# Optimization experiments

Measured on AMD Instinct MI355X. Metric: run time of the kernel, lower is better.

## Reference

```python
import jax, jax.numpy as jnp
import numpy as np

K = 5          # number of neighbors (topk k=5+1, drop self)
EPS = 1e-05    # hparams['epsilon'] for gentropy term


def setup_inputs() -> dict:
    key = jax.random.key(0)
    k1, k2, k3, k4, k5 = jax.random.split(key, 5)
    B, D, C, N = 256, 256, 64, 200000
    features = jax.random.normal(k1, (B, D), dtype=jnp.float32)
    W = jax.random.normal(k2, (D, C), dtype=jnp.float32) * 0.05
    b = jnp.zeros((C,), dtype=jnp.float32)
    fea_bank = jax.random.normal(k3, (N, D), dtype=jnp.float32)
    # score bank holds softmax outputs -> make rows valid probability distributions
    score_bank = jax.nn.softmax(jax.random.normal(k4, (N, C), dtype=jnp.float32), axis=-1)
    trg_idx = jax.random.randint(k5, (B,), 0, N, dtype=jnp.int64)
    return {"features": features, "W": W, "b": b,
            "fea_bank": fea_bank, "score_bank": score_bank, "trg_idx": trg_idx}


def reference(features, W, b, fea_bank, score_bank, trg_idx):
    sg = jax.lax.stop_gradient
    B = features.shape[0]
    C = W.shape[1]

    logits = features @ W + b                       # classifier(features)
    softmax_out = jax.nn.softmax(logits, axis=-1)   # [B, C] (differentiable)

    # --- everything bank-related is under torch.no_grad in the original ---
    nrm = jnp.maximum(jnp.linalg.norm(features, axis=1, keepdims=True), 1e-12)
    f_norm = sg(features / nrm)                     # F.normalize(features)
    fb = sg(fea_bank.at[trg_idx].set(f_norm))        # fea_bank[trg_idx] = f_norm
    sb = sg(score_bank.at[trg_idx].set(sg(softmax_out)))

    dist = f_norm @ fb.T                             # [B, N]
    _, idx_near = jax.lax.top_k(dist, K + 1)
    idx_near = idx_near[:, 1:]                       # [B, K] drop self

    score_near = sb[idx_near]                        # [B, K, C]
    fea_near = fb[idx_near]                          # [B, K, D]

    dist2 = jnp.einsum('bkd,nd->bkn', fea_near, fb)  # [B, K, N]
    _, idx_nn = jax.lax.top_k(dist2, K + 1)
    idx_nn = idx_nn[:, :, 1:]                        # [B, K, K]

    match = (idx_nn == trg_idx[:, None, None]).sum(-1).astype(jnp.float32)  # [B, K]
    weight = jnp.where(match > 0.0, match, jnp.float32(0.1))                # [B, K]
    weight_kk = jnp.full((B, K * K), 0.1, dtype=jnp.float32)  # fill_(0.1) overwrites

    score_near_kk = sb[idx_nn].reshape(B, K * K, C)  # [B, K*K, C]
    # --- end no_grad region ---

    # F.kl_div(input, target, reduction='none') = target * (log(target) - input)
    # (original passes probabilities, not log-probs, as input -- kept faithfully)
    kl_kk = score_near_kk * (jnp.log(score_near_kk) - softmax_out[:, None, :])
    loss = jnp.mean((kl_kk.sum(-1) * weight_kk).sum(1))

    kl_n = score_near * (jnp.log(score_near) - softmax_out[:, None, :])
    loss = loss + jnp.mean((kl_n.sum(-1) * weight).sum(1))

    msoftmax = softmax_out.mean(axis=0)
    gentropy = jnp.sum(msoftmax * jnp.log(msoftmax + EPS))
    loss = loss + gentropy
    return loss
```

## Files before the change

kernel.cpp:

```cpp
#include <hip/hip_runtime.h>
#include <hip/hip_bf16.h>
#include <math.h>

#define B_SZ   256
#define D_DIM  256
#define C_DIM  64
#define N_CAND 200000
#define K_TOP  5
#define CHUNK  64
#define NCHGLB (N_CAND / CHUNK)
#define CHUNK_SH 16384
#define NCHJ1  8
#define NCHJ2  16
#define S1     ((NCHGLB + NCHJ1 - 1) / NCHJ1)
#define S2     ((NCHGLB + NCHJ2 - 1) / NCHJ2)

typedef short bf16x8 __attribute__((ext_vector_type(8)));
typedef float f32x16 __attribute__((ext_vector_type(16)));
typedef unsigned short u16x8 __attribute__((ext_vector_type(8)));

__device__ __forceinline__ bool better(float v1, int i1, float v2, int i2) {
    return (v1 > v2) || (v1 == v2 && i1 < i2);
}

__device__ __forceinline__ void insert6f(float* lv, int* li, float v, int idx) {
    if (better(v, idx, lv[5], li[5])) {
        lv[5] = v; li[5] = idx;
        #pragma unroll
        for (int k = 5; k > 0; --k) {
            if (better(lv[k], li[k], lv[k - 1], li[k - 1])) {
                float tv = lv[k]; lv[k] = lv[k - 1]; lv[k - 1] = tv;
                int   ti = li[k]; li[k] = li[k - 1]; li[k - 1] = ti;
            }
        }
    }
}

__device__ __forceinline__ void merge6(const float* av, const int* ai,
                                       const float* bv, const int* bi,
                                       float* ov, int* oi) {
    int ia = 0, ib = 0;
    #pragma unroll
    for (int k = 0; k < 6; ++k) {
        bool ta;
        if (ia >= 6)      ta = false;
        else if (ib >= 6) ta = true;
        else              ta = better(av[ia], ai[ia], bv[ib], bi[ib]);
        if (ta) { ov[k] = av[ia]; oi[k] = ai[ia]; ++ia; }
        else    { ov[k] = bv[ib]; oi[k] = bi[ib]; ++ib; }
    }
}

__device__ __forceinline__ unsigned med3u(unsigned a, unsigned b, unsigned c) {
    unsigned d;
    asm("v_med3_u32 %0, %1, %2, %3" : "=v"(d) : "v"(a), "v"(b), "v"(c));
    return d;
}

__device__ __forceinline__ void kinsert(unsigned* kv, unsigned x) {
    unsigned n0 = kv[0] > x ? kv[0] : x;
    unsigned n1 = med3u(x, kv[0], kv[1]);
    unsigned n2 = med3u(x, kv[1], kv[2]);
    unsigned n3 = med3u(x, kv[2], kv[3]);
    unsigned n4 = med3u(x, kv[3], kv[4]);
    unsigned n5 = med3u(x, kv[4], kv[5]);
    kv[0] = n0; kv[1] = n1; kv[2] = n2; kv[3] = n3; kv[4] = n4; kv[5] = n5;
}

__device__ __forceinline__ unsigned short bf16rne(float x) {
    unsigned int u = __float_as_uint(x);
    unsigned int r = u + 0x7fffu + ((u >> 16) & 1u);
    return (unsigned short)(r >> 16);
}

__device__ __forceinline__ int perm_e(int r, int kk) {
    return ((kk >> 4) * 128) + ((r >> 5) * 64) + (((kk >> 3) & 1) * 32) + (r & 31);
}

__device__ __forceinline__ u16x8 pack8(float4 a, float4 b) {
    u16x8 h;
    h[0] = bf16rne(a.x); h[1] = bf16rne(a.y); h[2] = bf16rne(a.z); h[3] = bf16rne(a.w);
    h[4] = bf16rne(b.x); h[5] = bf16rne(b.y); h[6] = bf16rne(b.z); h[7] = bf16rne(b.w);
    return h;
}

__global__ void k_init(int* pos_of, float* accp) {
    int i = blockIdx.x * 256 + threadIdx.x;
    if (i < N_CAND) pos_of[i] = -1;
    if (i == 0) accp[0] = 0.f;
}

__global__ void k_scatter(const int* __restrict__ trg, int* __restrict__ pos_of) {
    int j = threadIdx.x;
    atomicMax(&pos_of[trg[j]], j);
}

__global__ __launch_bounds__(256) void k_prep(const float* __restrict__ features,
                                              const float* __restrict__ W,
                                              const float* __restrict__ bias,
                                              float* __restrict__ f_norm,
                                              float* __restrict__ softm) {
    int b = blockIdx.x, t = threadIdx.x;
    __shared__ float row[256];
    __shared__ float red[256];
    float x = features[b * D_DIM + t];
    row[t] = x; red[t] = x * x;
    __syncthreads();
    for (int s = 128; s > 0; s >>= 1) {
        if (t < s) red[t] += red[t + s];
        __syncthreads();
    }
    float nrm = fmaxf(sqrtf(red[0]), 1e-12f);
    f_norm[b * D_DIM + t] = x / nrm;
    if (t < C_DIM) {
        float acc = bias[t];
        for (int d = 0; d < D_DIM; ++d) acc = fmaf(row[d], W[d * C_DIM + t], acc);
        float mx = acc;
        for (int off = 32; off > 0; off >>= 1) mx = fmaxf(mx, __shfl_xor(mx, off, 64));
        float e = expf(acc - mx);
        float ssum = e;
        for (int off = 32; off > 0; off >>= 1) ssum += __shfl_xor(ssum, off, 64);
        softm[b * C_DIM + t] = e / ssum;
    }
}

__global__ __launch_bounds__(256) void k_convert(const float* __restrict__ fea_bank,
                                                 const float* __restrict__ f_norm,
                                                 const int* __restrict__ pos_of,
                                                 short* __restrict__ bank) {
    int cc = blockIdx.x, t = threadIdx.x;
    int r = t >> 2, q4 = t & 3;
    int n = cc * CHUNK + r;
    int p = pos_of[n];
    const float* src = (p >= 0) ? (f_norm + (size_t)p * D_DIM)
                                : (fea_bank + (size_t)n * D_DIM);
    short* dst = bank + (size_t)cc * CHUNK_SH;
    #pragma unroll
    for (int i = 0; i < 8; ++i) {
        int kk = q4 * 64 + i * 8;
        float4 a = *(const float4*)(src + kk);
        float4 b = *(const float4*)(src + kk + 4);
        *(u16x8*)(dst + (size_t)perm_e(r, kk) * 8) = pack8(a, b);
    }
}

__global__ __launch_bounds__(256) void k_permq(const float* __restrict__ rows,
                                               const float* __restrict__ fea_bank,
                                               const int* __restrict__ idx,
                                               const int* __restrict__ pos_of,
                                               short* __restrict__ dst) {
    int tile = blockIdx.x, t = threadIdx.x;
    int r = t >> 2, q4 = t & 3;
    const float* src;
    if (idx) {
        int n = idx[tile * 64 + r];
        int p = pos_of[n];
        src = (p >= 0) ? (rows + (size_t)p * D_DIM) : (fea_bank + (size_t)n * D_DIM);
    } else {
        src = rows + (size_t)(tile * 64 + r) * D_DIM;
    }
    short* d = dst + (size_t)tile * CHUNK_SH;
    #pragma unroll
    for (int i = 0; i < 8; ++i) {
        int kk = q4 * 64 + i * 8;
        float4 a = *(const float4*)(src + kk);
        float4 b = *(const float4*)(src + kk + 4);
        *(u16x8*)(d + (size_t)perm_e(r, kk) * 8) = pack8(a, b);
    }
}

__global__ __launch_bounds__(256, 2) void dist_topk(const short* __restrict__ qbf,
                                                    const short* __restrict__ bank,
                                                    float* __restrict__ pval,
                                                    int* __restrict__ pidx,
                                                    int nqt, int swz,
                                                    int S, int nchj) {
    __shared__ __align__(16) short sbuf[2 * CHUNK_SH];

    int slab, qt;
    if (swz) {
        int bid = blockIdx.x;
        int xcd = bid & 7;
        int rem = bid >> 3;
        qt = rem % nqt;
        slab = (rem / nqt) * 8 + xcd;
        if (slab >= S) return;
    } else {
        slab = blockIdx.x;
        qt = blockIdx.y;
    }
    const int cfirst = slab * nchj;
    int nch = NCHGLB - cfirst; if (nch > nchj) nch = nchj;

    const int t   = threadIdx.x;
    const int w   = t >> 6;
    const int l   = t & 63;
    const int khv = l >> 5;
    const int col = l & 31;

    const short* qtile = qbf + (size_t)(qt * 4 + w) * CHUNK_SH;
    bf16x8 bfr0[16], bfr1[16];
    #pragma unroll
    for (int ks = 0; ks < 16; ++ks) {
        bfr0[ks] = *(const bf16x8*)(qtile + (size_t)(ks * 128      + l) * 8);
        bfr1[ks] = *(const bf16x8*)(qtile + (size_t)(ks * 128 + 64 + l) * 8);
    }

    unsigned kv0[6], kv1[6];
    #pragma unroll
    for (int k = 0; k < 6; ++k) { kv0[k] = 0u; kv1[k] = 0u; }

    const short* sbase = bank + (size_t)cfirst * CHUNK_SH;

    #pragma unroll
    for (int i = 0; i < 8; ++i) {
        const short* gp = sbase + (size_t)(i * 256 + t) * 8;
        short* lp = sbuf + (size_t)(i * 256 + w * 64) * 8;
        __builtin_amdgcn_global_load_lds(
            (const __attribute__((address_space(1))) void*)gp,
            (__attribute__((address_space(3))) void*)lp, 16, 0, 0);
    }

    for (int ch = 0; ch < nch; ++ch) {
        const int cur = ch & 1;
        if (ch + 1 < nch) {
            const short* g = sbase + (size_t)(ch + 1) * CHUNK_SH;
            short* lbase = sbuf + (size_t)(cur ^ 1) * CHUNK_SH;
            #pragma unroll
            for (int i = 0; i < 8; ++i) {
                const short* gp = g + (size_t)(i * 256 + t) * 8;
                short* lp = lbase + (size_t)(i * 256 + w * 64) * 8;
                __builtin_amdgcn_global_load_lds(
                    (const __attribute__((address_space(1))) void*)gp,
                    (__attribute__((address_space(3))) void*)lp, 16, 0, 0);
            }
            asm volatile("s_waitcnt vmcnt(8)" ::: "memory");
        } else {
            asm volatile("s_waitcnt vmcnt(0)" ::: "memory");
        }
        __builtin_amdgcn_s_barrier();
        __builtin_amdgcn_sched_barrier(0);

        const short* cb = sbuf + (size_t)cur * CHUNK_SH;

        #pragma unroll
        for (int half = 0; half < 2; ++half) {
            f32x16 a0, a1;
            #pragma unroll
            for (int i = 0; i < 16; ++i) { a0[i] = 2.0f; a1[i] = 2.0f; }
            #pragma unroll
            for (int ks = 0; ks < 16; ++ks) {
                bf16x8 fa = *(const bf16x8*)(cb + (size_t)(ks * 128 + half * 64 + l) * 8);
                a0 = __builtin_amdgcn_mfma_f32_32x32x16_bf16(fa, bfr0[ks], a0, 0, 0, 0);
                a1 = __builtin_amdgcn_mfma_f32_32x32x16_bf16(fa, bfr1[ks], a1, 0, 0, 0);
            }

            const unsigned invb = 511u - (unsigned)(ch * 32 + half * 16);
            #pragma unroll
            for (int r = 0; r < 16; ++r) {
                unsigned x0 = (__float_as_uint(a0[r]) & 0xFFFFFE00u) | (invb - r);
                unsigned x1 = (__float_as_uint(a1[r]) & 0xFFFFFE00u) | (invb - r);
                kinsert(kv0, x0);
                kinsert(kv1, x1);
            }
        }

        __builtin_amdgcn_sched_barrier(0);
        __builtin_amdgcn_s_barrier();
    }

    {
        int q0 = qt * 256 + w * 64 + col;
        int q1 = qt * 256 + w * 64 + 32 + col;
        size_t b0 = ((size_t)q0 * S + slab) * 12 + khv * 6;
        size_t b1 = ((size_t)q1 * S + slab) * 12 + khv * 6;
        #pragma unroll
        for (int k = 0; k < 6; ++k) {
            unsigned key0 = kv0[k], key1 = kv1[k];
            int pos0 = 511 - (int)(key0 & 511u);
            int pos1 = 511 - (int)(key1 & 511u);
            int r0 = pos0 & 15, h0 = (pos0 >> 4) & 1, c0 = pos0 >> 5;
            int r1 = pos1 & 15, h1 = (pos1 >> 4) & 1, c1 = pos1 >> 5;
            int m0 = (r0 & 3) + 8 * (r0 >> 2) + 4 * khv;
            int m1 = (r1 & 3) + 8 * (r1 >> 2) + 4 * khv;
            pval[b0 + k] = __uint_as_float(key0 & 0xFFFFFE00u);
            pidx[b0 + k] = (cfirst + c0) * CHUNK + h0 * 32 + m0;
            pval[b1 + k] = __uint_as_float(key1 & 0xFFFFFE00u);
            pidx[b1 + k] = (cfirst + c1) * CHUNK + h1 * 32 + m1;
        }
    }
}

__global__ __launch_bounds__(256) void topk_merge(const float* __restrict__ pval,
                                                  const int* __restrict__ pidx,
                                                  int* __restrict__ out_idx,
                                                  int S) {
    int q = blockIdx.x, t = threadIdx.x;
    const int total = S * 12;
    float lv[6]; int li[6];
    #pragma unroll
    for (int k = 0; k < 6; ++k) { lv[k] = -3.4e38f; li[k] = 0x7fffffff; }
    size_t base = (size_t)q * total;
    for (int e = t; e < total; e += 256) insert6f(lv, li, pval[base + e], pidx[base + e]);
    __shared__ float sv[256][6];
    __shared__ int   si[256][6];
    #pragma unroll
    for (int k = 0; k < 6; ++k) { sv[t][k] = lv[k]; si[t][k] = li[k]; }
    __syncthreads();
    for (int w = 128; w >= 1; w >>= 1) {
        if (t < w) {
            float ov[6]; int oi[6];
            merge6(sv[t], si[t], sv[t + w], si[t + w], ov, oi);
            #pragma unroll
            for (int k = 0; k < 6; ++k) { sv[t][k] = ov[k]; si[t][k] = oi[k]; }
        }
        __syncthreads();
    }
    if (t == 0) {
        for (int k = 1; k < 6; ++k) out_idx[q * K_TOP + k - 1] = si[0][k];
    }
}

__global__ void k_loss(const float* __restrict__ softm, const float* __restrict__ score_bank,
                       const int* __restrict__ pos_of, const int* __restrict__ idx_near,
                       const int* __restrict__ idx_nn, const int* __restrict__ trg,
                       float* accp) {
    int b = blockIdx.x, c = threadIdx.x;
    float p_bc = softm[b * C_DIM + c];
    float part = 0.f;
    for (int k = 0; k < K_TOP; ++k) {
        for (int j = 0; j < K_TOP; ++j) {
            int n = idx_nn[(b * K_TOP + k) * K_TOP + j];
            int p = pos_of[n];
            const float* srow = (p >= 0) ? (softm + (size_t)p * C_DIM)
                                         : (score_bank + (size_t)n * C_DIM);
            float s = srow[c];
            float v = s * (logf(s) - p_bc);
            for (int off = 32; off > 0; off >>= 1) v += __shfl_down(v, off, 64);
            if (c == 0) part += 0.1f * v;
        }
    }
    for (int k = 0; k < K_TOP; ++k) {
        int n = idx_near[b * K_TOP + k];
        int p = pos_of[n];
        const float* srow = (p >= 0) ? (softm + (size_t)p * C_DIM)
                                     : (score_bank + (size_t)n * C_DIM);
        float s = srow[c];
        float v = s * (logf(s) - p_bc);
        for (int off = 32; off > 0; off >>= 1) v += __shfl_down(v, off, 64);
        if (c == 0) {
            int m = 0;
            for (int j = 0; j < K_TOP; ++j)
                m += (idx_nn[(b * K_TOP + k) * K_TOP + j] == trg[b]) ? 1 : 0;
            float w = (m > 0) ? (float)m : 0.1f;
            part += w * v;
        }
    }
    if (c == 0) atomicAdd(accp, part * (1.0f / (float)B_SZ));
}

__global__ void k_final(const float* __restrict__ softm, const float* __restrict__ accp,
                        float* __restrict__ out) {
    int c = threadIdx.x;
    float m = 0.f;
    for (int b = 0; b < B_SZ; ++b) m += softm[b * C_DIM + c];
    m *= (1.0f / (float)B_SZ);
    float g = m * logf(m + 1e-5f);
    for (int off = 32; off > 0; off >>= 1) g += __shfl_down(g, off, 64);
    if (c == 0) out[0] = accp[0] + g;
}

extern "C" void kernel_launch(void* const* d_in, const int* in_sizes, int n_in,
                              void* d_out, int out_size, void* d_ws, size_t ws_size,
                              hipStream_t stream) {
    const float* features   = (const float*)d_in[0];
    const float* W          = (const float*)d_in[1];
    const float* bias       = (const float*)d_in[2];
    const float* fea_bank   = (const float*)d_in[3];
    const float* score_bank = (const float*)d_in[4];
    const int*   trg        = (const int*)d_in[5];
    float* out = (float*)d_out;

    char* ws = (char*)d_ws;
    size_t off = 0;
    auto alloc = [&](size_t bytes) -> void* {
        void* p = ws + off;
        off = (off + bytes + 255) & ~(size_t)255;
        return p;
    };
    short* bankbf   = (short*)alloc((size_t)NCHGLB * CHUNK_SH * 2);
    short* q1bf     = (short*)alloc((size_t)(B_SZ / 64) * CHUNK_SH * 2);
    short* q2bf     = (short*)alloc((size_t)(B_SZ * K_TOP / 64) * CHUNK_SH * 2);
    float* f_norm   = (float*)alloc((size_t)B_SZ * D_DIM * 4);
    float* softm    = (float*)alloc((size_t)B_SZ * C_DIM * 4);
    int*   pos_of   = (int*)alloc((size_t)N_CAND * 4);
    float* accp     = (float*)alloc(4);
    int*   idx_near = (int*)alloc((size_t)B_SZ * K_TOP * 4);
    int*   idx_nn   = (int*)alloc((size_t)B_SZ * K_TOP * K_TOP * 4);
    float* pv1      = (float*)alloc((size_t)B_SZ * S1 * 12 * 4);
    int*   pi1      = (int*)alloc((size_t)B_SZ * S1 * 12 * 4);
    float* pv2      = (float*)alloc((size_t)B_SZ * K_TOP * S2 * 12 * 4);
    int*   pi2      = (int*)alloc((size_t)B_SZ * K_TOP * S2 * 12 * 4);

    k_init<<<dim3((N_CAND + 255) / 256), dim3(256), 0, stream>>>(pos_of, accp);
    k_scatter<<<dim3(1), dim3(256), 0, stream>>>(trg, pos_of);
    k_prep<<<dim3(B_SZ), dim3(256), 0, stream>>>(features, W, bias, f_norm, softm);

    k_convert<<<dim3(NCHGLB), dim3(256), 0, stream>>>(fea_bank, f_norm, pos_of, bankbf);
    k_permq<<<dim3(B_SZ / 64), dim3(256), 0, stream>>>(f_norm, fea_bank, nullptr, pos_of, q1bf);

    dist_topk<<<dim3(S1, 1), dim3(256), 0, stream>>>(
        q1bf, bankbf, pv1, pi1, 1, 0, S1, NCHJ1);
    topk_merge<<<dim3(B_SZ), dim3(256), 0, stream>>>(pv1, pi1, idx_near, S1);

    k_permq<<<dim3(B_SZ * K_TOP / 64), dim3(256), 0, stream>>>(
        f_norm, fea_bank, idx_near, pos_of, q2bf);

    {
        int nqt = (B_SZ * K_TOP) / 256;
        int nsg = (S2 + 7) / 8;
        dist_topk<<<dim3(nsg * 8 * nqt), dim3(256), 0, stream>>>(
            q2bf, bankbf, pv2, pi2, nqt, 1, S2, NCHJ2);
    }
    topk_merge<<<dim3(B_SZ * K_TOP), dim3(256), 0, stream>>>(pv2, pi2, idx_nn, S2);

    k_loss<<<dim3(B_SZ), dim3(64), 0, stream>>>(softm, score_bank, pos_of, idx_near, idx_nn, trg, accp);
    k_final<<<dim3(1), dim3(64), 0, stream>>>(softm, accp, out);
}
```

Measured before the change: 342.1 us.

## Halve candidate chunk and per-wave query tile to raise dist_topk occupancy

Shrinks the bank chunk from 64 to 32 candidates and gives each wave 32 queries instead of 64, so each wave runs one accumulator and one top-k list. Register and LDS use per block drop, and launch bounds move from 2 to 4 blocks per CU. Slabs and query tiles are reorganized so twice as many blocks cover the same work. In exchange, each staged bank chunk is now reused by half as many queries per block, which increases LDS and L2 traffic per MFMA. The bank layout and the index encoding are changed to match.

Result: faster. 331.9 us (-3.0%).

```diff
diff --git a/kernel.cpp b/kernel.cpp
--- a/kernel.cpp
+++ b/kernel.cpp
@@ -7,13 +7,14 @@
 #define C_DIM  64
 #define N_CAND 200000
 #define K_TOP  5
-#define CHUNK  64
-#define NCHGLB (N_CAND / CHUNK)
-#define CHUNK_SH 16384
-#define NCHJ1  8
-#define NCHJ2  16
-#define S1     ((NCHGLB + NCHJ1 - 1) / NCHJ1)
-#define S2     ((NCHGLB + NCHJ2 - 1) / NCHJ2)
+#define CH32   32
+#define CH32_SH 8192
+#define QTILE_SH 16384
+#define NCH32  (N_CAND / CH32)
+#define NCHJ1  16
+#define NCHJ2  32
+#define S1     ((NCH32 + NCHJ1 - 1) / NCHJ1)
+#define S2     ((NCH32 + NCHJ2 - 1) / NCHJ2)
 
 typedef short bf16x8 __attribute__((ext_vector_type(8)));
 typedef float f32x16 __attribute__((ext_vector_type(16)));
@@ -71,10 +72,6 @@
     unsigned int u = __float_as_uint(x);
     unsigned int r = u + 0x7fffu + ((u >> 16) & 1u);
     return (unsigned short)(r >> 16);
-}
-
-__device__ __forceinline__ int perm_e(int r, int kk) {
-    return ((kk >> 4) * 128) + ((r >> 5) * 64) + (((kk >> 3) & 1) * 32) + (r & 31);
 }
 
 __device__ __forceinline__ u16x8 pack8(float4 a, float4 b) {
@@ -130,17 +127,19 @@
                                                  short* __restrict__ bank) {
     int cc = blockIdx.x, t = threadIdx.x;
     int r = t >> 2, q4 = t & 3;
-    int n = cc * CHUNK + r;
+    int n = cc * 64 + r;
     int p = pos_of[n];
     const float* src = (p >= 0) ? (f_norm + (size_t)p * D_DIM)
                                 : (fea_bank + (size_t)n * D_DIM);
-    short* dst = bank + (size_t)cc * CHUNK_SH;
+    short* dst = bank + (size_t)(cc * 2 + (r >> 5)) * CH32_SH;
+    int rl = r & 31;
     #pragma unroll
     for (int i = 0; i < 8; ++i) {
         int kk = q4 * 64 + i * 8;
         float4 a = *(const float4*)(src + kk);
         float4 b = *(const float4*)(src + kk + 4);
-        *(u16x8*)(dst + (size_t)perm_e(r, kk) * 8) = pack8(a, b);
+        int e = ((kk >> 4) * 64) + (((kk >> 3) & 1) * 32) + rl;
+        *(u16x8*)(dst + (size_t)e * 8) = pack8(a, b);
     }
 }
 
@@ -159,23 +158,24 @@
     } else {
         src = rows + (size_t)(tile * 64 + r) * D_DIM;
     }
-    short* d = dst + (size_t)tile * CHUNK_SH;
+    short* d = dst + (size_t)tile * QTILE_SH;
     #pragma unroll
     for (int i = 0; i < 8; ++i) {
         int kk = q4 * 64 + i * 8;
         float4 a = *(const float4*)(src + kk);
         float4 b = *(const float4*)(src + kk + 4);
-        *(u16x8*)(d + (size_t)perm_e(r, kk) * 8) = pack8(a, b);
-    }
-}
-
-__global__ __launch_bounds__(256, 2) void dist_topk(const short* __restrict__ qbf,
+        int e = ((kk >> 4) * 128) + ((r >> 5) * 64) + (((kk >> 3) & 1) * 32) + (r & 31);
+        *(u16x8*)(d + (size_t)e * 8) = pack8(a, b);
+    }
+}
+
+__global__ __launch_bounds__(256, 4) void dist_topk(const short* __restrict__ qbf,
                                                     const short* __restrict__ bank,
                                                     float* __restrict__ pval,
                                                     int* __restrict__ pidx,
                                                     int nqt, int swz,
                                                     int S, int nchj) {
-    __shared__ __align__(16) short sbuf[2 * CHUNK_SH];
+    __shared__ __align__(16) short sbuf[2 * CH32_SH];
 
     int slab, qt;
     if (swz) {
@@ -190,7 +190,7 @@
         qt = blockIdx.y;
     }
     const int cfirst = slab * nchj;
-    int nch = NCHGLB - cfirst; if (nch > nchj) nch = nchj;
+    int nch = NCH32 - cfirst; if (nch > nchj) nch = nchj;
 
     const int t   = threadIdx.x;
     const int w   = t >> 6;
@@ -198,22 +198,21 @@
     const int khv = l >> 5;
     const int col = l & 31;
 
-    const short* qtile = qbf + (size_t)(qt * 4 + w) * CHUNK_SH;
-    bf16x8 bfr0[16], bfr1[16];
-    #pragma unroll
-    for (int ks = 0; ks < 16; ++ks) {
-        bfr0[ks] = *(const bf16x8*)(qtile + (size_t)(ks * 128      + l) * 8);
-        bfr1[ks] = *(const bf16x8*)(qtile + (size_t)(ks * 128 + 64 + l) * 8);
-    }
-
-    unsigned kv0[6], kv1[6];
-    #pragma unroll
-    for (int k = 0; k < 6; ++k) { kv0[k] = 0u; kv1[k] = 0u; }
-
-    const short* sbase = bank + (size_t)cfirst * CHUNK_SH;
-
-    #pragma unroll
-    for (int i = 0; i < 8; ++i) {
+    const short* qtile = qbf + (size_t)(qt * 2 + (w >> 1)) * QTILE_SH;
+    const int half = w & 1;
+    bf16x8 bfr[16];
+    #pragma unroll
+    for (int ks = 0; ks < 16; ++ks)
+        bfr[ks] = *(const bf16x8*)(qtile + (size_t)(ks * 128 + half * 64 + l) * 8);
+
+    unsigned kv[6];
+    #pragma unroll
+    for (int k = 0; k < 6; ++k) kv[k] = 0u;
+
+    const short* sbase = bank + (size_t)cfirst * CH32_SH;
+
+    #pragma unroll
+    for (int i = 0; i < 4; ++i) {
         const short* gp = sbase + (size_t)(i * 256 + t) * 8;
         short* lp = sbuf + (size_t)(i * 256 + w * 64) * 8;
         __builtin_amdgcn_global_load_lds(
@@ -224,45 +223,40 @@
     for (int ch = 0; ch < nch; ++ch) {
         const int cur = ch & 1;
         if (ch + 1 < nch) {
-            const short* g = sbase + (size_t)(ch + 1) * CHUNK_SH;
-            short* lbase = sbuf + (size_t)(cur ^ 1) * CHUNK_SH;
+            const short* g = sbase + (size_t)(ch + 1) * CH32_SH;
+            short* lbase = sbuf + (size_t)(cur ^ 1) * CH32_SH;
             #pragma unroll
-            for (int i = 0; i < 8; ++i) {
+            for (int i = 0; i < 4; ++i) {
                 const short* gp = g + (size_t)(i * 256 + t) * 8;
                 short* lp = lbase + (size_t)(i * 256 + w * 64) * 8;
                 __builtin_amdgcn_global_load_lds(
                     (const __attribute__((address_space(1))) void*)gp,
                     (__attribute__((address_space(3))) void*)lp, 16, 0, 0);
             }
-            asm volatile("s_waitcnt vmcnt(8)" ::: "memory");
+            asm volatile("s_waitcnt vmcnt(4)" ::: "memory");
         } else {
             asm volatile("s_waitcnt vmcnt(0)" ::: "memory");
         }
         __builtin_amdgcn_s_barrier();
         __builtin_amdgcn_sched_barrier(0);
 
-        const short* cb = sbuf + (size_t)cur * CHUNK_SH;
-
+        const short* cb = sbuf + (size_t)cur * CH32_SH;
+
+        f32x16 a;
         #pragma unroll
-        for (int half = 0; half < 2; ++half) {
-            f32x16 a0, a1;
-            #pragma unroll
-            for (int i = 0; i < 16; ++i) { a0[i] = 2.0f; a1[i] = 2.0f; }
-            #pragma unroll
-            for (int ks = 0; ks < 16; ++ks) {
-                bf16x8 fa = *(const bf16x8*)(cb + (size_t)(ks * 128 + half * 64 + l) * 8);
-                a0 = __builtin_amdgcn_mfma_f32_32x32x16_bf16(fa, bfr0[ks], a0, 0, 0, 0);
-                a1 = __builtin_amdgcn_mfma_f32_32x32x16_bf16(fa, bfr1[ks], a1, 0, 0, 0);
-            }
-
-            const unsigned invb = 511u - (unsigned)(ch * 32 + half * 16);
-            #pragma unroll
-            for (int r = 0; r < 16; ++r) {
-                unsigned x0 = (__float_as_uint(a0[r]) & 0xFFFFFE00u) | (invb - r);
-                unsigned x1 = (__float_as_uint(a1[r]) & 0xFFFFFE00u) | (invb - r);
-                kinsert(kv0, x0);
-                kinsert(kv1, x1);
-            }
+        for (int i = 0; i < 16; ++i) a[i] = 2.0f;
+        #pragma unroll
+        for (int ks = 0; ks < 16; ++ks) {
+            bf16x8 fa = *(const bf16x8*)(cb + (size_t)(ks * 64 + l) * 8);
+            a = __builtin_amdgcn_mfma_f32_32x32x16_bf16(fa, bfr[ks], a, 0, 0, 0);
+        }
+
+        const unsigned invb = 1023u - (unsigned)(ch * 32);
+        #pragma unroll
+        for (int r = 0; r < 16; ++r) {
+            unsigned m = (unsigned)((r & 3) + 8 * (r >> 2) + 4 * khv);
+            unsigned x = (__float_as_uint(a[r]) & 0xFFFFFC00u) | (invb - m);
+            kinsert(kv, x);
         }
 
         __builtin_amdgcn_sched_barrier(0);
@@ -270,23 +264,15 @@
     }
 
     {
-        int q0 = qt * 256 + w * 64 + col;
-        int q1 = qt * 256 + w * 64 + 32 + col;
-        size_t b0 = ((size_t)q0 * S + slab) * 12 + khv * 6;
-        size_t b1 = ((size_t)q1 * S + slab) * 12 + khv * 6;
+        int q = qt * 128 + w * 32 + col;
+        size_t b0 = ((size_t)q * S + slab) * 12 + khv * 6;
         #pragma unroll
         for (int k = 0; k < 6; ++k) {
-            unsigned key0 = kv0[k], key1 = kv1[k];
-            int pos0 = 511 - (int)(key0 & 511u);
-            int pos1 = 511 - (int)(key1 & 511u);
-            int r0 = pos0 & 15, h0 = (pos0 >> 4) & 1, c0 = pos0 >> 5;
-            int r1 = pos1 & 15, h1 = (pos1 >> 4) & 1, c1 = pos1 >> 5;
-            int m0 = (r0 & 3) + 8 * (r0 >> 2) + 4 * khv;
-            int m1 = (r1 & 3) + 8 * (r1 >> 2) + 4 * khv;
-            pval[b0 + k] = __uint_as_float(key0 & 0xFFFFFE00u);
-            pidx[b0 + k] = (cfirst + c0) * CHUNK + h0 * 32 + m0;
-            pval[b1 + k] = __uint_as_float(key1 & 0xFFFFFE00u);
-            pidx[b1 + k] = (cfirst + c1) * CHUNK + h1 * 32 + m1;
+            unsigned key = kv[k];
+            int pos = 1023 - (int)(key & 1023u);
+            int c = pos >> 5, m = pos & 31;
+            pval[b0 + k] = __uint_as_float(key & 0xFFFFFC00u);
+            pidx[b0 + k] = (cfirst + c) * CH32 + m;
         }
     }
 }
@@ -388,9 +374,9 @@
         off = (off + bytes + 255) & ~(size_t)255;
         return p;
     };
-    short* bankbf   = (short*)alloc((size_t)NCHGLB * CHUNK_SH * 2);
-    short* q1bf     = (short*)alloc((size_t)(B_SZ / 64) * CHUNK_SH * 2);
-    short* q2bf     = (short*)alloc((size_t)(B_SZ * K_TOP / 64) * CHUNK_SH * 2);
+    short* bankbf   = (short*)alloc((size_t)NCH32 * CH32_SH * 2);
+    short* q1bf     = (short*)alloc((size_t)(B_SZ / 64) * QTILE_SH * 2);
+    short* q2bf     = (short*)alloc((size_t)(B_SZ * K_TOP / 64) * QTILE_SH * 2);
     float* f_norm   = (float*)alloc((size_t)B_SZ * D_DIM * 4);
     float* softm    = (float*)alloc((size_t)B_SZ * C_DIM * 4);
     int*   pos_of   = (int*)alloc((size_t)N_CAND * 4);
@@ -406,18 +392,18 @@
     k_scatter<<<dim3(1), dim3(256), 0, stream>>>(trg, pos_of);
     k_prep<<<dim3(B_SZ), dim3(256), 0, stream>>>(features, W, bias, f_norm, softm);
 
-    k_convert<<<dim3(NCHGLB), dim3(256), 0, stream>>>(fea_bank, f_norm, pos_of, bankbf);
+    k_convert<<<dim3(NCH32 / 2), dim3(256), 0, stream>>>(fea_bank, f_norm, pos_of, bankbf);
     k_permq<<<dim3(B_SZ / 64), dim3(256), 0, stream>>>(f_norm, fea_bank, nullptr, pos_of, q1bf);
 
-    dist_topk<<<dim3(S1, 1), dim3(256), 0, stream>>>(
-        q1bf, bankbf, pv1, pi1, 1, 0, S1, NCHJ1);
+    dist_topk<<<dim3(S1, 2), dim3(256), 0, stream>>>(
+        q1bf, bankbf, pv1, pi1, 2, 0, S1, NCHJ1);
     topk_merge<<<dim3(B_SZ), dim3(256), 0, stream>>>(pv1, pi1, idx_near, S1);
 
     k_permq<<<dim3(B_SZ * K_TOP / 64), dim3(256), 0, stream>>>(
         f_norm, fea_bank, idx_near, pos_of, q2bf);
 
     {
-        int nqt = (B_SZ * K_TOP) / 256;
+        int nqt = (B_SZ * K_TOP) / 128;
         int nsg = (S2 + 7) / 8;
         dist_topk<<<dim3(nsg * 8 * nqt), dim3(256), 0, stream>>>(
             q2bf, bankbf, pv2, pi2, nqt, 1, S2, NCHJ2);
```
